# Kernel tuning notes

Measured on AMD Instinct MI355X. Metric: run time of the kernel, lower is better.

## Reference

```python
import jax, jax.numpy as jnp
import numpy as np


def setup_inputs() -> dict:
    key = jax.random.key(0)
    k1, k2, k3, k4 = jax.random.split(key, 4)
    B, S, IN, OUT = 2, 2048, 2048, 4096
    C, K, V = 128, 16, 16  # ncodebooks, ncentroids, vec_len
    return {
        "x": jax.random.normal(k1, (B, S, IN), dtype=jnp.float32),
        "weight": jax.random.normal(k2, (IN, OUT), dtype=jnp.float32) * 0.02,
        "centroids": jax.random.normal(k3, (C, K * V), dtype=jnp.float32),
        "bias": jax.random.normal(k4, (OUT,), dtype=jnp.float32) * 0.01,
        "vec_len": V,
    }


def reference(x, weight, centroids, bias, vec_len):
    B, S, IN = x.shape
    C = centroids.shape[0]            # ncodebooks
    V = vec_len
    K = centroids.shape[1] // V       # ncentroids
    OUT = weight.shape[1]
    N = B * S

    # [C, N, V] per-codebook token sub-vectors
    x_flat = jnp.transpose(x.reshape(N, C, V), (1, 0, 2))
    # [C, V, OUT] per-codebook weight slabs
    w_flat = weight.reshape(C, V, OUT)

    # soft path: sum_c x_c @ W_c  (fused contraction, no [C,N,OUT] intermediate)
    soft = jnp.einsum('cnv,cvo->no', x_flat, w_flat)

    # distance (p = inf -> Chebyshev) and nearest-centroid selection
    cents = centroids.reshape(C, K, V)
    dist = jnp.max(jnp.abs(x_flat[:, :, None, :] - cents[:, None, :, :]), axis=-1)  # [C,N,K]
    min_indices = jnp.argmin(dist, axis=-1)  # [C,N]

    # LUT: centroid outputs per codebook, then gather (== one_hot @ lut)
    lut = jnp.einsum('ckv,cvo->cko', cents, w_flat)  # [C,K,OUT]
    quant = jnp.sum(lut[jnp.arange(C)[:, None], min_indices], axis=0)  # [N,OUT]

    # straight-through estimator
    out = soft + jax.lax.stop_gradient(quant - soft)
    out = out.reshape(B, S, OUT) + bias
    return out
```

## Files before the change

### kernel.cpp

```cpp
#include <hip/hip_runtime.h>

typedef unsigned int u32;
typedef unsigned long long u64;
typedef __bf16 bf16x8 __attribute__((ext_vector_type(8)));
typedef float f32x4 __attribute__((ext_vector_type(4)));

#define N_TOK 4096
#define IN_DIM 2048
#define OUT_DIM 4096
#define NCB 128
#define NCENT 16
#define VLEN 16
#define CK 2048
#define KB 64

static __device__ __forceinline__ unsigned short f2bf(float f) {
  u32 u = __float_as_uint(f);
  u = (u + 0x7FFFu + ((u >> 16) & 1u)) >> 16;
  return (unsigned short)u;
}

__global__ __launch_bounds__(256) void k_argmin_idx(
    const float* __restrict__ x,
    const float* __restrict__ cents,
    unsigned char* __restrict__ idx) {
  __shared__ float xs[16 * 260];
  __shared__ float cs[16 * 260];
  const int tid = threadIdx.x;
  const int n0 = blockIdx.x * 16;
  const int t = tid >> 4;
  const int cl = tid & 15;

  for (int g = 0; g < 4; ++g) {
    const int cg = blockIdx.y * 4 + g;
#pragma unroll
    for (int j = 0; j < 4; ++j) {
      const int fi = tid + 256 * j;
      const int row = fi >> 6;
      const int col = (fi & 63) * 4;
      *(float4*)(xs + row * 260 + col) =
          *(const float4*)(x + (size_t)(n0 + row) * IN_DIM + cg * 256 + col);
      *(float4*)(cs + row * 260 + col) =
          *(const float4*)(cents + ((size_t)cg * 16 + row) * 256 + col);
    }
    __syncthreads();

    float xr[16];
    const float* xv = xs + t * 260 + cl * 16;
#pragma unroll
    for (int q = 0; q < 4; ++q) {
      float4 tv = *(const float4*)(xv + q * 4);
      xr[q * 4 + 0] = tv.x; xr[q * 4 + 1] = tv.y;
      xr[q * 4 + 2] = tv.z; xr[q * 4 + 3] = tv.w;
    }
    const float* cb = cs + cl * 260;
    int bk = 0;
    float bd = 1e30f;
#pragma unroll
    for (int k = 0; k < NCENT; ++k) {
      float d = 0.f;
#pragma unroll
      for (int v = 0; v < VLEN; ++v) d = fmaxf(d, fabsf(xr[v] - cb[k * 16 + v]));
      if (d < bd) { bd = d; bk = k; }
    }
    idx[(size_t)(n0 + t) * NCB + cg * 16 + cl] = (unsigned char)bk;
    __syncthreads();
  }
}

__global__ __launch_bounds__(256) void k_lut(const float* __restrict__ w,
                                             const float* __restrict__ cents,
                                             char* __restrict__ lutF) {
  const int tid = threadIdx.x;
  const int o0 = blockIdx.x * 64;
  const int cg = blockIdx.y;
  const int p = tid >> 6;
  const int ol = tid & 63;
  const int o = o0 + ol;

  float acc[2][16];
#pragma unroll
  for (int cc = 0; cc < 2; ++cc)
#pragma unroll
    for (int k = 0; k < 16; ++k) acc[cc][k] = 0.f;

#pragma unroll
  for (int cc = 0; cc < 2; ++cc) {
    const int c = __builtin_amdgcn_readfirstlane(cg * 8 + p * 2 + cc);
    const float* cb = cents + (size_t)c * (NCENT * VLEN);
#pragma unroll
    for (int v = 0; v < VLEN; ++v) {
      const float wv = w[(size_t)(c * 16 + v) * OUT_DIM + o];
#pragma unroll
      for (int k = 0; k < NCENT; ++k) acc[cc][k] = fmaf(cb[k * 16 + v], wv, acc[cc][k]);
    }
  }

#pragma unroll
  for (int cc = 0; cc < 2; ++cc) {
    const int c = cg * 8 + p * 2 + cc;
    u32 g[8];
#pragma unroll
    for (int kk = 0; kk < 8; ++kk)
      g[kk] = (u32)f2bf(acc[cc][2 * kk]) | ((u32)f2bf(acc[cc][2 * kk + 1]) << 16);
    char* base = lutF + ((size_t)(o >> 4) * KB + (c >> 1)) * 1024;
    const int l0 = (o & 15) + ((c & 1) * 2) * 16;
    *(uint4*)(base + l0 * 16)        = make_uint4(g[0], g[1], g[2], g[3]);
    *(uint4*)(base + (l0 + 16) * 16) = make_uint4(g[4], g[5], g[6], g[7]);
  }
}

__global__ __launch_bounds__(256) void k_gemm(
    const unsigned char* __restrict__ idx,
    const char* __restrict__ Bf,
    const float* __restrict__ bias,
    float* __restrict__ out) {
  __shared__ unsigned char sIdx[128 * 144];
  const int tid = threadIdx.x;
  const int wave = tid >> 6;
  const int lane = tid & 63;

  const int lin = blockIdx.x + (int)(gridDim.x * blockIdx.y);
  const int slot = lin >> 3;
  const int bx = slot & 31;
  const int by = ((lin & 7) << 2) | (slot >> 5);
  const int m0 = bx * 128;
  const int n0 = by * 128;
  const int wm = (wave >> 1) * 64;
  const int wn = (wave & 1) * 64;

#pragma unroll
  for (int j = 0; j < 4; ++j) {
    const int u = tid + 256 * j;
    const int row = u >> 3;
    const int col = (u & 7) * 16;
    *(uint4*)(sIdx + row * 144 + col) =
        *(const uint4*)(idx + (size_t)(m0 + row) * NCB + col);
  }

  const int h = lane >> 4;
  const int hb = h >> 1;
  const u32 par8 = (u32)((h & 1) * 8);
  const u32 sh0 = (u32)(hb * 8);
  const u32 sh1 = sh0 + 16;
  const unsigned char* rb[4];
#pragma unroll
  for (int i = 0; i < 4; ++i) rb[i] = sIdx + (wm + i * 16 + (lane & 15)) * 144;

  const int tb = (n0 >> 4) + (wn >> 4);
  u32 bo0 = (u32)tb * (KB * 1024) + (u32)lane * 16;
  u32 bo1 = bo0 + KB * 1024;
  u32 bo2 = bo1 + KB * 1024;
  u32 bo3 = bo2 + KB * 1024;

  __syncthreads();

  uint4 Bc0 = *(const uint4*)(Bf + bo0);
  uint4 Bc1 = *(const uint4*)(Bf + bo1);
  uint4 Bc2 = *(const uint4*)(Bf + bo2);
  uint4 Bc3 = *(const uint4*)(Bf + bo3);
  bo0 += 1024; bo1 += 1024; bo2 += 1024; bo3 += 1024;

  f32x4 acc[4][4] = {};

  for (int q = 0; q < 8; ++q) {
    uint4 ch[4];
#pragma unroll
    for (int i = 0; i < 4; ++i) ch[i] = *(const uint4*)(rb[i] + q * 16);

#pragma unroll
    for (int j = 0; j < 8; ++j) {
      uint4 Bn0 = *(const uint4*)(Bf + bo0);
      uint4 Bn1 = *(const uint4*)(Bf + bo1);
      uint4 Bn2 = *(const uint4*)(Bf + bo2);
      uint4 Bn3 = *(const uint4*)(Bf + bo3);
      bo0 += 1024; bo1 += 1024; bo2 += 1024; bo3 += 1024;

      const u32 sh = (j & 1) ? sh1 : sh0;
      bf16x8 af[4];
#pragma unroll
      for (int i = 0; i < 4; ++i) {
        const u32 word = (j >> 1) == 0 ? ch[i].x
                       : (j >> 1) == 1 ? ch[i].y
                       : (j >> 1) == 2 ? ch[i].z
                                       : ch[i].w;
        const u32 iv = (word >> sh) & 0xFu;
        const u32 uu = iv ^ par8;
        const u64 dbl = 0x3F80ull << ((uu & 3u) << 4);
        const u64 lo = ((uu & 12u) == 0u) ? dbl : 0ull;
        const u64 hi = ((uu & 12u) == 4u) ? dbl : 0ull;
        uint4 f;
        f.x = (u32)lo; f.y = (u32)(lo >> 32);
        f.z = (u32)hi; f.w = (u32)(hi >> 32);
        af[i] = *(bf16x8*)&f;
      }

#pragma unroll
      for (int i = 0; i < 4; ++i) {
        acc[i][0] = __builtin_amdgcn_mfma_f32_16x16x32_bf16(
            af[i], *(const bf16x8*)&Bc0, acc[i][0], 0, 0, 0);
        acc[i][1] = __builtin_amdgcn_mfma_f32_16x16x32_bf16(
            af[i], *(const bf16x8*)&Bc1, acc[i][1], 0, 0, 0);
        acc[i][2] = __builtin_amdgcn_mfma_f32_16x16x32_bf16(
            af[i], *(const bf16x8*)&Bc2, acc[i][2], 0, 0, 0);
        acc[i][3] = __builtin_amdgcn_mfma_f32_16x16x32_bf16(
            af[i], *(const bf16x8*)&Bc3, acc[i][3], 0, 0, 0);
      }

      Bc0 = Bn0; Bc1 = Bn1; Bc2 = Bn2; Bc3 = Bn3;
    }
  }

  const int col = lane & 15;
  const int rbq = (lane >> 4) * 4;
  float bj[4];
#pragma unroll
  for (int j = 0; j < 4; ++j) bj[j] = bias[n0 + wn + j * 16 + col];
#pragma unroll
  for (int i = 0; i < 4; ++i) {
    const int gm = m0 + wm + i * 16 + rbq;
#pragma unroll
    for (int j = 0; j < 4; ++j) {
      const int gn = n0 + wn + j * 16 + col;
      float* op = out + (size_t)gm * OUT_DIM + gn;
#pragma unroll
      for (int r = 0; r < 4; ++r) op[(size_t)r * OUT_DIM] = acc[i][j][r] + bj[j];
    }
  }
}

extern "C" void kernel_launch(void* const* d_in, const int* in_sizes, int n_in,
                              void* d_out, int out_size, void* d_ws, size_t ws_size,
                              hipStream_t stream) {
  (void)in_sizes; (void)n_in; (void)out_size; (void)ws_size;
  const float* x      = (const float*)d_in[0];
  const float* weight = (const float*)d_in[1];
  const float* cents  = (const float*)d_in[2];
  const float* bias   = (const float*)d_in[3];

  char* lutF = (char*)d_ws;
  unsigned char* idx = (unsigned char*)d_ws + (size_t)OUT_DIM * CK * 2;
  float* out = (float*)d_out;

  k_argmin_idx<<<dim3(N_TOK / 16, 2), 256, 0, stream>>>(x, cents, idx);
  k_lut<<<dim3(OUT_DIM / 64, NCB / 8), 256, 0, stream>>>(weight, cents, lutF);
  k_gemm<<<dim3(N_TOK / 128, OUT_DIM / 128), 256, 0, stream>>>(idx, lutF, bias, out);
}
```

Baseline: 190.2 us.

## Fuse LUT and argmin prep kernels, retile GEMM waves to 32x128 strips

Merges the LUT build and the nearest-centroid search into a single launch whose first 1024 blocks build the LUT and whose remaining blocks compute argmin indices. The argmin part now has each thread handle two tokens, reading x directly from global memory, and spreads the work over more blocks. The GEMM gives each wave a 32-row by 128-column strip instead of 64x64. This cuts per-wave one-hot A-fragment construction in half, moves the parity XOR out of the inner loop, and reuses each A fragment across 8 B tiles. The cost is more B-fragment registers and global loads per wave, which may lower occupancy.

```diff
diff --git a/kernel.cpp b/kernel.cpp
--- a/kernel.cpp
+++ b/kernel.cpp
@@ -20,94 +20,106 @@
   return (unsigned short)u;
 }
 
-__global__ __launch_bounds__(256) void k_argmin_idx(
+__global__ __launch_bounds__(256) void k_prep(
     const float* __restrict__ x,
+    const float* __restrict__ w,
     const float* __restrict__ cents,
-    unsigned char* __restrict__ idx) {
-  __shared__ float xs[16 * 260];
+    unsigned char* __restrict__ idx,
+    char* __restrict__ lutF) {
   __shared__ float cs[16 * 260];
   const int tid = threadIdx.x;
-  const int n0 = blockIdx.x * 16;
+  const int b = blockIdx.x;
+
+  if (b < 1024) {
+    const int o0 = (b & 63) * 64;
+    const int cg = b >> 6;
+    const int p = tid >> 6;
+    const int ol = tid & 63;
+    const int o = o0 + ol;
+
+    float acc[2][16];
+#pragma unroll
+    for (int cc = 0; cc < 2; ++cc)
+#pragma unroll
+      for (int k = 0; k < 16; ++k) acc[cc][k] = 0.f;
+
+#pragma unroll
+    for (int cc = 0; cc < 2; ++cc) {
+      const int c = __builtin_amdgcn_readfirstlane(cg * 8 + p * 2 + cc);
+      const float* cb = cents + (size_t)c * (NCENT * VLEN);
+#pragma unroll
+      for (int v = 0; v < VLEN; ++v) {
+        const float wv = w[(size_t)(c * 16 + v) * OUT_DIM + o];
+#pragma unroll
+        for (int k = 0; k < 16; ++k) acc[cc][k] = fmaf(cb[k * 16 + v], wv, acc[cc][k]);
+      }
+    }
+
+#pragma unroll
+    for (int cc = 0; cc < 2; ++cc) {
+      const int c = cg * 8 + p * 2 + cc;
+      u32 g[8];
+#pragma unroll
+      for (int kk = 0; kk < 8; ++kk)
+        g[kk] = (u32)f2bf(acc[cc][2 * kk]) | ((u32)f2bf(acc[cc][2 * kk + 1]) << 16);
+      char* base = lutF + ((size_t)(o >> 4) * KB + (c >> 1)) * 1024;
+      const int l0 = (o & 15) + ((c & 1) * 2) * 16;
+      *(uint4*)(base + l0 * 16)        = make_uint4(g[0], g[1], g[2], g[3]);
+      *(uint4*)(base + (l0 + 16) * 16) = make_uint4(g[4], g[5], g[6], g[7]);
+    }
+    return;
+  }
+
+  const int a = b - 1024;
+  const int n0 = (a & 127) * 32;
+  const int cg = a >> 7;
   const int t = tid >> 4;
   const int cl = tid & 15;
 
-  for (int g = 0; g < 4; ++g) {
-    const int cg = blockIdx.y * 4 + g;
-#pragma unroll
-    for (int j = 0; j < 4; ++j) {
-      const int fi = tid + 256 * j;
-      const int row = fi >> 6;
-      const int col = (fi & 63) * 4;
-      *(float4*)(xs + row * 260 + col) =
-          *(const float4*)(x + (size_t)(n0 + row) * IN_DIM + cg * 256 + col);
-      *(float4*)(cs + row * 260 + col) =
-          *(const float4*)(cents + ((size_t)cg * 16 + row) * 256 + col);
-    }
-    __syncthreads();
-
-    float xr[16];
-    const float* xv = xs + t * 260 + cl * 16;
-#pragma unroll
-    for (int q = 0; q < 4; ++q) {
-      float4 tv = *(const float4*)(xv + q * 4);
-      xr[q * 4 + 0] = tv.x; xr[q * 4 + 1] = tv.y;
-      xr[q * 4 + 2] = tv.z; xr[q * 4 + 3] = tv.w;
-    }
-    const float* cb = cs + cl * 260;
-    int bk = 0;
-    float bd = 1e30f;
-#pragma unroll
-    for (int k = 0; k < NCENT; ++k) {
-      float d = 0.f;
-#pragma unroll
-      for (int v = 0; v < VLEN; ++v) d = fmaxf(d, fabsf(xr[v] - cb[k * 16 + v]));
-      if (d < bd) { bd = d; bk = k; }
-    }
-    idx[(size_t)(n0 + t) * NCB + cg * 16 + cl] = (unsigned char)bk;
-    __syncthreads();
-  }
-}
-
-__global__ __launch_bounds__(256) void k_lut(const float* __restrict__ w,
-                                             const float* __restrict__ cents,
-                                             char* __restrict__ lutF) {
-  const int tid = threadIdx.x;
-  const int o0 = blockIdx.x * 64;
-  const int cg = blockIdx.y;
-  const int p = tid >> 6;
-  const int ol = tid & 63;
-  const int o = o0 + ol;
-
-  float acc[2][16];
-#pragma unroll
-  for (int cc = 0; cc < 2; ++cc)
-#pragma unroll
-    for (int k = 0; k < 16; ++k) acc[cc][k] = 0.f;
-
-#pragma unroll
-  for (int cc = 0; cc < 2; ++cc) {
-    const int c = __builtin_amdgcn_readfirstlane(cg * 8 + p * 2 + cc);
-    const float* cb = cents + (size_t)c * (NCENT * VLEN);
-#pragma unroll
-    for (int v = 0; v < VLEN; ++v) {
-      const float wv = w[(size_t)(c * 16 + v) * OUT_DIM + o];
-#pragma unroll
-      for (int k = 0; k < NCENT; ++k) acc[cc][k] = fmaf(cb[k * 16 + v], wv, acc[cc][k]);
-    }
-  }
-
-#pragma unroll
-  for (int cc = 0; cc < 2; ++cc) {
-    const int c = cg * 8 + p * 2 + cc;
-    u32 g[8];
-#pragma unroll
-    for (int kk = 0; kk < 8; ++kk)
-      g[kk] = (u32)f2bf(acc[cc][2 * kk]) | ((u32)f2bf(acc[cc][2 * kk + 1]) << 16);
-    char* base = lutF + ((size_t)(o >> 4) * KB + (c >> 1)) * 1024;
-    const int l0 = (o & 15) + ((c & 1) * 2) * 16;
-    *(uint4*)(base + l0 * 16)        = make_uint4(g[0], g[1], g[2], g[3]);
-    *(uint4*)(base + (l0 + 16) * 16) = make_uint4(g[4], g[5], g[6], g[7]);
-  }
+#pragma unroll
+  for (int j2 = 0; j2 < 4; ++j2) {
+    const int fi = tid + 256 * j2;
+    const int row = fi >> 6;
+    const int col = (fi & 63) * 4;
+    *(float4*)(cs + row * 260 + col) =
+        *(const float4*)(cents + ((size_t)(cg * 16 + row)) * 256 + col);
+  }
+
+  float xr[2][16];
+#pragma unroll
+  for (int s = 0; s < 2; ++s)
+#pragma unroll
+    for (int qq = 0; qq < 4; ++qq) {
+      float4 tv = *(const float4*)(x + (size_t)(n0 + t + 16 * s) * IN_DIM +
+                                   cg * 256 + cl * 16 + qq * 4);
+      xr[s][qq * 4 + 0] = tv.x; xr[s][qq * 4 + 1] = tv.y;
+      xr[s][qq * 4 + 2] = tv.z; xr[s][qq * 4 + 3] = tv.w;
+    }
+  __syncthreads();
+
+  const float* cb = cs + cl * 260;
+  int bk0 = 0, bk1 = 0;
+  float bd0 = 1e30f, bd1 = 1e30f;
+#pragma unroll
+  for (int k = 0; k < 16; ++k) {
+    float d0 = 0.f, d1 = 0.f;
+#pragma unroll
+    for (int qq = 0; qq < 4; ++qq) {
+      float4 cv = *(const float4*)(cb + k * 16 + qq * 4);
+      d0 = fmaxf(d0, fabsf(xr[0][qq * 4 + 0] - cv.x));
+      d0 = fmaxf(d0, fabsf(xr[0][qq * 4 + 1] - cv.y));
+      d0 = fmaxf(d0, fabsf(xr[0][qq * 4 + 2] - cv.z));
+      d0 = fmaxf(d0, fabsf(xr[0][qq * 4 + 3] - cv.w));
+      d1 = fmaxf(d1, fabsf(xr[1][qq * 4 + 0] - cv.x));
+      d1 = fmaxf(d1, fabsf(xr[1][qq * 4 + 1] - cv.y));
+      d1 = fmaxf(d1, fabsf(xr[1][qq * 4 + 2] - cv.z));
+      d1 = fmaxf(d1, fabsf(xr[1][qq * 4 + 3] - cv.w));
+    }
+    if (d0 < bd0) { bd0 = d0; bk0 = k; }
+    if (d1 < bd1) { bd1 = d1; bk1 = k; }
+  }
+  idx[(size_t)(n0 + t) * NCB + cg * 16 + cl] = (unsigned char)bk0;
+  idx[(size_t)(n0 + t + 16) * NCB + cg * 16 + cl] = (unsigned char)bk1;
 }
 
 __global__ __launch_bounds__(256) void k_gemm(
@@ -126,8 +138,7 @@
   const int by = ((lin & 7) << 2) | (slot >> 5);
   const int m0 = bx * 128;
   const int n0 = by * 128;
-  const int wm = (wave >> 1) * 64;
-  const int wn = (wave & 1) * 64;
+  const int wm = wave * 32;
 
 #pragma unroll
   for (int j = 0; j < 4; ++j) {
@@ -139,92 +150,87 @@
   }
 
   const int h = lane >> 4;
-  const int hb = h >> 1;
-  const u32 par8 = (u32)((h & 1) * 8);
-  const u32 sh0 = (u32)(hb * 8);
-  const u32 sh1 = sh0 + 16;
-  const unsigned char* rb[4];
-#pragma unroll
-  for (int i = 0; i < 4; ++i) rb[i] = sIdx + (wm + i * 16 + (lane & 15)) * 144;
-
-  const int tb = (n0 >> 4) + (wn >> 4);
-  u32 bo0 = (u32)tb * (KB * 1024) + (u32)lane * 16;
-  u32 bo1 = bo0 + KB * 1024;
-  u32 bo2 = bo1 + KB * 1024;
-  u32 bo3 = bo2 + KB * 1024;
+  const u32 sh_e = (u32)((h >> 1) * 8);
+  const u32 sh_o = sh_e + 16u;
+  const u32 pxor = (h & 1) ? 0x08080808u : 0u;
+  const unsigned char* rb0 = sIdx + (wm + (lane & 15)) * 144;
+  const unsigned char* rb1 = rb0 + 16 * 144;
+
+  u32 bo[8];
+#pragma unroll
+  for (int jj = 0; jj < 8; ++jj)
+    bo[jj] = (u32)(((n0 >> 4) + jj) * (KB * 1024)) + (u32)lane * 16u;
 
   __syncthreads();
 
-  uint4 Bc0 = *(const uint4*)(Bf + bo0);
-  uint4 Bc1 = *(const uint4*)(Bf + bo1);
-  uint4 Bc2 = *(const uint4*)(Bf + bo2);
-  uint4 Bc3 = *(const uint4*)(Bf + bo3);
-  bo0 += 1024; bo1 += 1024; bo2 += 1024; bo3 += 1024;
-
-  f32x4 acc[4][4] = {};
+  uint4 Bc[8];
+#pragma unroll
+  for (int jj = 0; jj < 8; ++jj) Bc[jj] = *(const uint4*)(Bf + bo[jj]);
+
+  f32x4 acc[2][8] = {};
 
   for (int q = 0; q < 8; ++q) {
-    uint4 ch[4];
-#pragma unroll
-    for (int i = 0; i < 4; ++i) ch[i] = *(const uint4*)(rb[i] + q * 16);
+    uint4 c0 = *(const uint4*)(rb0 + q * 16);
+    uint4 c1 = *(const uint4*)(rb1 + q * 16);
+    c0.x ^= pxor; c0.y ^= pxor; c0.z ^= pxor; c0.w ^= pxor;
+    c1.x ^= pxor; c1.y ^= pxor; c1.z ^= pxor; c1.w ^= pxor;
 
 #pragma unroll
     for (int j = 0; j < 8; ++j) {
-      uint4 Bn0 = *(const uint4*)(Bf + bo0);
-      uint4 Bn1 = *(const uint4*)(Bf + bo1);
-      uint4 Bn2 = *(const uint4*)(Bf + bo2);
-      uint4 Bn3 = *(const uint4*)(Bf + bo3);
-      bo0 += 1024; bo1 += 1024; bo2 += 1024; bo3 += 1024;
-
-      const u32 sh = (j & 1) ? sh1 : sh0;
-      bf16x8 af[4];
-#pragma unroll
-      for (int i = 0; i < 4; ++i) {
-        const u32 word = (j >> 1) == 0 ? ch[i].x
-                       : (j >> 1) == 1 ? ch[i].y
-                       : (j >> 1) == 2 ? ch[i].z
-                                       : ch[i].w;
-        const u32 iv = (word >> sh) & 0xFu;
-        const u32 uu = iv ^ par8;
-        const u64 dbl = 0x3F80ull << ((uu & 3u) << 4);
-        const u64 lo = ((uu & 12u) == 0u) ? dbl : 0ull;
-        const u64 hi = ((uu & 12u) == 4u) ? dbl : 0ull;
-        uint4 f;
-        f.x = (u32)lo; f.y = (u32)(lo >> 32);
-        f.z = (u32)hi; f.w = (u32)(hi >> 32);
-        af[i] = *(bf16x8*)&f;
+      uint4 Bn[8];
+#pragma unroll
+      for (int jj = 0; jj < 8; ++jj)
+        Bn[jj] = *(const uint4*)(Bf + (bo[jj] + (u32)((j + 1) * 1024)));
+
+      const u32 w0 = ((j >> 1) == 0 ? c0.x : (j >> 1) == 1 ? c0.y
+                     : (j >> 1) == 2 ? c0.z : c0.w);
+      const u32 w1 = ((j >> 1) == 0 ? c1.x : (j >> 1) == 1 ? c1.y
+                     : (j >> 1) == 2 ? c1.z : c1.w);
+      const u32 sh = (j & 1) ? sh_o : sh_e;
+      const u32 uu0 = (w0 >> sh) & 15u;
+      const u32 uu1 = (w1 >> sh) & 15u;
+      const u64 dbl0 = 0x3F80ull << ((uu0 << 4) & 63u);
+      const u64 dbl1 = 0x3F80ull << ((uu1 << 4) & 63u);
+      const u64 lo0 = (uu0 < 4u) ? dbl0 : 0ull;
+      const u64 hi0 = (uu0 >= 4u && uu0 < 8u) ? dbl0 : 0ull;
+      const u64 lo1 = (uu1 < 4u) ? dbl1 : 0ull;
+      const u64 hi1 = (uu1 >= 4u && uu1 < 8u) ? dbl1 : 0ull;
+      uint4 f0, f1;
+      f0.x = (u32)lo0; f0.y = (u32)(lo0 >> 32);
+      f0.z = (u32)hi0; f0.w = (u32)(hi0 >> 32);
+      f1.x = (u32)lo1; f1.y = (u32)(lo1 >> 32);
+      f1.z = (u32)hi1; f1.w = (u32)(hi1 >> 32);
+      const bf16x8 af0 = *(const bf16x8*)&f0;
+      const bf16x8 af1 = *(const bf16x8*)&f1;
+
+#pragma unroll
+      for (int jj = 0; jj < 8; ++jj) {
+        acc[0][jj] = __builtin_amdgcn_mfma_f32_16x16x32_bf16(
+            af0, *(const bf16x8*)&Bc[jj], acc[0][jj], 0, 0, 0);
+        acc[1][jj] = __builtin_amdgcn_mfma_f32_16x16x32_bf16(
+            af1, *(const bf16x8*)&Bc[jj], acc[1][jj], 0, 0, 0);
       }
 
 #pragma unroll
-      for (int i = 0; i < 4; ++i) {
-        acc[i][0] = __builtin_amdgcn_mfma_f32_16x16x32_bf16(
-            af[i], *(const bf16x8*)&Bc0, acc[i][0], 0, 0, 0);
-        acc[i][1] = __builtin_amdgcn_mfma_f32_16x16x32_bf16(
-            af[i], *(const bf16x8*)&Bc1, acc[i][1], 0, 0, 0);
-        acc[i][2] = __builtin_amdgcn_mfma_f32_16x16x32_bf16(
-            af[i], *(const bf16x8*)&Bc2, acc[i][2], 0, 0, 0);
-        acc[i][3] = __builtin_amdgcn_mfma_f32_16x16x32_bf16(
-            af[i], *(const bf16x8*)&Bc3, acc[i][3], 0, 0, 0);
-      }
-
-      Bc0 = Bn0; Bc1 = Bn1; Bc2 = Bn2; Bc3 = Bn3;
-    }
+      for (int jj = 0; jj < 8; ++jj) Bc[jj] = Bn[jj];
+    }
+#pragma unroll
+    for (int jj = 0; jj < 8; ++jj) bo[jj] += 8192u;
   }
 
   const int col = lane & 15;
-  const int rbq = (lane >> 4) * 4;
-  float bj[4];
-#pragma unroll
-  for (int j = 0; j < 4; ++j) bj[j] = bias[n0 + wn + j * 16 + col];
-#pragma unroll
-  for (int i = 0; i < 4; ++i) {
-    const int gm = m0 + wm + i * 16 + rbq;
-#pragma unroll
-    for (int j = 0; j < 4; ++j) {
-      const int gn = n0 + wn + j * 16 + col;
-      float* op = out + (size_t)gm * OUT_DIM + gn;
-#pragma unroll
-      for (int r = 0; r < 4; ++r) op[(size_t)r * OUT_DIM] = acc[i][j][r] + bj[j];
+  const int rq = (lane >> 4) * 4;
+  float bj[8];
+#pragma unroll
+  for (int jj = 0; jj < 8; ++jj) bj[jj] = bias[n0 + jj * 16 + col];
+#pragma unroll
+  for (int i = 0; i < 2; ++i) {
+    const int gm = m0 + wm + i * 16 + rq;
+#pragma unroll
+    for (int jj = 0; jj < 8; ++jj) {
+      float* op = out + (size_t)gm * OUT_DIM + n0 + jj * 16 + col;
+#pragma unroll
+      for (int r = 0; r < 4; ++r) op[(size_t)r * OUT_DIM] = acc[i][jj][r] + bj[jj];
     }
   }
 }
@@ -242,7 +248,6 @@
   unsigned char* idx = (unsigned char*)d_ws + (size_t)OUT_DIM * CK * 2;
   float* out = (float*)d_out;
 
-  k_argmin_idx<<<dim3(N_TOK / 16, 2), 256, 0, stream>>>(x, cents, idx);
-  k_lut<<<dim3(OUT_DIM / 64, NCB / 8), 256, 0, stream>>>(weight, cents, lutF);
-  k_gemm<<<dim3(N_TOK / 128, OUT_DIM / 128), 256, 0, stream>>>(idx, lutF, bias, out);
-}
+  k_prep<<<dim3(2048), 256, 0, stream>>>(x, weight, cents, idx, lutF);
+  k_gemm<<<dim3(32, 32), 256, 0, stream>>>(idx, lutF, bias, out);
+}
```

Result: slower. 206.0 us (+8.3%).

## Merge argmin and LUT kernels into one launch and simplify one-hot decode

Applied to the files above, without the earlier changes.

Combines the LUT-building kernel and the nearest-centroid argmin kernel into one launch using a block-index split, which removes one kernel launch and lets the two independent stages run concurrently. The argmin path now has each thread handle two tokens per codebook and reads x straight from global memory, so the x shared-memory staging is gone and more blocks run in parallel. In the GEMM, the parity XOR is applied once per loaded index word rather than on every decode, and the one-hot construction uses cheaper comparisons. The risk is load imbalance between the two block types sharing one grid.

```diff
diff --git a/kernel.cpp b/kernel.cpp
--- a/kernel.cpp
+++ b/kernel.cpp
@@ -20,94 +20,106 @@
   return (unsigned short)u;
 }
 
-__global__ __launch_bounds__(256) void k_argmin_idx(
+__global__ __launch_bounds__(256) void k_prep(
     const float* __restrict__ x,
+    const float* __restrict__ w,
     const float* __restrict__ cents,
-    unsigned char* __restrict__ idx) {
-  __shared__ float xs[16 * 260];
+    unsigned char* __restrict__ idx,
+    char* __restrict__ lutF) {
   __shared__ float cs[16 * 260];
   const int tid = threadIdx.x;
-  const int n0 = blockIdx.x * 16;
+  const int b = blockIdx.x;
+
+  if (b < 1024) {
+    const int o0 = (b & 63) * 64;
+    const int cg = b >> 6;
+    const int p = tid >> 6;
+    const int ol = tid & 63;
+    const int o = o0 + ol;
+
+    float acc[2][16];
+#pragma unroll
+    for (int cc = 0; cc < 2; ++cc)
+#pragma unroll
+      for (int k = 0; k < 16; ++k) acc[cc][k] = 0.f;
+
+#pragma unroll
+    for (int cc = 0; cc < 2; ++cc) {
+      const int c = __builtin_amdgcn_readfirstlane(cg * 8 + p * 2 + cc);
+      const float* cb = cents + (size_t)c * (NCENT * VLEN);
+#pragma unroll
+      for (int v = 0; v < VLEN; ++v) {
+        const float wv = w[(size_t)(c * 16 + v) * OUT_DIM + o];
+#pragma unroll
+        for (int k = 0; k < 16; ++k) acc[cc][k] = fmaf(cb[k * 16 + v], wv, acc[cc][k]);
+      }
+    }
+
+#pragma unroll
+    for (int cc = 0; cc < 2; ++cc) {
+      const int c = cg * 8 + p * 2 + cc;
+      u32 g[8];
+#pragma unroll
+      for (int kk = 0; kk < 8; ++kk)
+        g[kk] = (u32)f2bf(acc[cc][2 * kk]) | ((u32)f2bf(acc[cc][2 * kk + 1]) << 16);
+      char* base = lutF + ((size_t)(o >> 4) * KB + (c >> 1)) * 1024;
+      const int l0 = (o & 15) + ((c & 1) * 2) * 16;
+      *(uint4*)(base + l0 * 16)        = make_uint4(g[0], g[1], g[2], g[3]);
+      *(uint4*)(base + (l0 + 16) * 16) = make_uint4(g[4], g[5], g[6], g[7]);
+    }
+    return;
+  }
+
+  const int a = b - 1024;
+  const int n0 = (a & 127) * 32;
+  const int cg = a >> 7;
   const int t = tid >> 4;
   const int cl = tid & 15;
 
-  for (int g = 0; g < 4; ++g) {
-    const int cg = blockIdx.y * 4 + g;
-#pragma unroll
-    for (int j = 0; j < 4; ++j) {
-      const int fi = tid + 256 * j;
-      const int row = fi >> 6;
-      const int col = (fi & 63) * 4;
-      *(float4*)(xs + row * 260 + col) =
-          *(const float4*)(x + (size_t)(n0 + row) * IN_DIM + cg * 256 + col);
-      *(float4*)(cs + row * 260 + col) =
-          *(const float4*)(cents + ((size_t)cg * 16 + row) * 256 + col);
-    }
-    __syncthreads();
-
-    float xr[16];
-    const float* xv = xs + t * 260 + cl * 16;
-#pragma unroll
-    for (int q = 0; q < 4; ++q) {
-      float4 tv = *(const float4*)(xv + q * 4);
-      xr[q * 4 + 0] = tv.x; xr[q * 4 + 1] = tv.y;
-      xr[q * 4 + 2] = tv.z; xr[q * 4 + 3] = tv.w;
-    }
-    const float* cb = cs + cl * 260;
-    int bk = 0;
-    float bd = 1e30f;
-#pragma unroll
-    for (int k = 0; k < NCENT; ++k) {
-      float d = 0.f;
-#pragma unroll
-      for (int v = 0; v < VLEN; ++v) d = fmaxf(d, fabsf(xr[v] - cb[k * 16 + v]));
-      if (d < bd) { bd = d; bk = k; }
-    }
-    idx[(size_t)(n0 + t) * NCB + cg * 16 + cl] = (unsigned char)bk;
-    __syncthreads();
-  }
-}
-
-__global__ __launch_bounds__(256) void k_lut(const float* __restrict__ w,
-                                             const float* __restrict__ cents,
-                                             char* __restrict__ lutF) {
-  const int tid = threadIdx.x;
-  const int o0 = blockIdx.x * 64;
-  const int cg = blockIdx.y;
-  const int p = tid >> 6;
-  const int ol = tid & 63;
-  const int o = o0 + ol;
-
-  float acc[2][16];
-#pragma unroll
-  for (int cc = 0; cc < 2; ++cc)
-#pragma unroll
-    for (int k = 0; k < 16; ++k) acc[cc][k] = 0.f;
-
-#pragma unroll
-  for (int cc = 0; cc < 2; ++cc) {
-    const int c = __builtin_amdgcn_readfirstlane(cg * 8 + p * 2 + cc);
-    const float* cb = cents + (size_t)c * (NCENT * VLEN);
-#pragma unroll
-    for (int v = 0; v < VLEN; ++v) {
-      const float wv = w[(size_t)(c * 16 + v) * OUT_DIM + o];
-#pragma unroll
-      for (int k = 0; k < NCENT; ++k) acc[cc][k] = fmaf(cb[k * 16 + v], wv, acc[cc][k]);
-    }
-  }
-
-#pragma unroll
-  for (int cc = 0; cc < 2; ++cc) {
-    const int c = cg * 8 + p * 2 + cc;
-    u32 g[8];
-#pragma unroll
-    for (int kk = 0; kk < 8; ++kk)
-      g[kk] = (u32)f2bf(acc[cc][2 * kk]) | ((u32)f2bf(acc[cc][2 * kk + 1]) << 16);
-    char* base = lutF + ((size_t)(o >> 4) * KB + (c >> 1)) * 1024;
-    const int l0 = (o & 15) + ((c & 1) * 2) * 16;
-    *(uint4*)(base + l0 * 16)        = make_uint4(g[0], g[1], g[2], g[3]);
-    *(uint4*)(base + (l0 + 16) * 16) = make_uint4(g[4], g[5], g[6], g[7]);
-  }
+#pragma unroll
+  for (int j2 = 0; j2 < 4; ++j2) {
+    const int fi = tid + 256 * j2;
+    const int row = fi >> 6;
+    const int col = (fi & 63) * 4;
+    *(float4*)(cs + row * 260 + col) =
+        *(const float4*)(cents + ((size_t)(cg * 16 + row)) * 256 + col);
+  }
+
+  float xr[2][16];
+#pragma unroll
+  for (int s = 0; s < 2; ++s)
+#pragma unroll
+    for (int qq = 0; qq < 4; ++qq) {
+      float4 tv = *(const float4*)(x + (size_t)(n0 + t + 16 * s) * IN_DIM +
+                                   cg * 256 + cl * 16 + qq * 4);
+      xr[s][qq * 4 + 0] = tv.x; xr[s][qq * 4 + 1] = tv.y;
+      xr[s][qq * 4 + 2] = tv.z; xr[s][qq * 4 + 3] = tv.w;
+    }
+  __syncthreads();
+
+  const float* cb = cs + cl * 260;
+  int bk0 = 0, bk1 = 0;
+  float bd0 = 1e30f, bd1 = 1e30f;
+#pragma unroll
+  for (int k = 0; k < 16; ++k) {
+    float d0 = 0.f, d1 = 0.f;
+#pragma unroll
+    for (int qq = 0; qq < 4; ++qq) {
+      float4 cv = *(const float4*)(cb + k * 16 + qq * 4);
+      d0 = fmaxf(d0, fabsf(xr[0][qq * 4 + 0] - cv.x));
+      d0 = fmaxf(d0, fabsf(xr[0][qq * 4 + 1] - cv.y));
+      d0 = fmaxf(d0, fabsf(xr[0][qq * 4 + 2] - cv.z));
+      d0 = fmaxf(d0, fabsf(xr[0][qq * 4 + 3] - cv.w));
+      d1 = fmaxf(d1, fabsf(xr[1][qq * 4 + 0] - cv.x));
+      d1 = fmaxf(d1, fabsf(xr[1][qq * 4 + 1] - cv.y));
+      d1 = fmaxf(d1, fabsf(xr[1][qq * 4 + 2] - cv.z));
+      d1 = fmaxf(d1, fabsf(xr[1][qq * 4 + 3] - cv.w));
+    }
+    if (d0 < bd0) { bd0 = d0; bk0 = k; }
+    if (d1 < bd1) { bd1 = d1; bk1 = k; }
+  }
+  idx[(size_t)(n0 + t) * NCB + cg * 16 + cl] = (unsigned char)bk0;
+  idx[(size_t)(n0 + t + 16) * NCB + cg * 16 + cl] = (unsigned char)bk1;
 }
 
 __global__ __launch_bounds__(256) void k_gemm(
@@ -139,16 +151,15 @@
   }
 
   const int h = lane >> 4;
-  const int hb = h >> 1;
-  const u32 par8 = (u32)((h & 1) * 8);
-  const u32 sh0 = (u32)(hb * 8);
-  const u32 sh1 = sh0 + 16;
+  const u32 sh_e = (u32)((h >> 1) * 8);
+  const u32 sh_o = sh_e + 16u;
+  const u32 pxor = (h & 1) ? 0x08080808u : 0u;
   const unsigned char* rb[4];
 #pragma unroll
   for (int i = 0; i < 4; ++i) rb[i] = sIdx + (wm + i * 16 + (lane & 15)) * 144;
 
   const int tb = (n0 >> 4) + (wn >> 4);
-  u32 bo0 = (u32)tb * (KB * 1024) + (u32)lane * 16;
+  u32 bo0 = (u32)(tb + 0) * (KB * 1024) + (u32)lane * 16;
   u32 bo1 = bo0 + KB * 1024;
   u32 bo2 = bo1 + KB * 1024;
   u32 bo3 = bo2 + KB * 1024;
@@ -166,7 +177,10 @@
   for (int q = 0; q < 8; ++q) {
     uint4 ch[4];
 #pragma unroll
-    for (int i = 0; i < 4; ++i) ch[i] = *(const uint4*)(rb[i] + q * 16);
+    for (int i = 0; i < 4; ++i) {
+      ch[i] = *(const uint4*)(rb[i] + q * 16);
+      ch[i].x ^= pxor; ch[i].y ^= pxor; ch[i].z ^= pxor; ch[i].w ^= pxor;
+    }
 
 #pragma unroll
     for (int j = 0; j < 8; ++j) {
@@ -176,7 +190,7 @@
       uint4 Bn3 = *(const uint4*)(Bf + bo3);
       bo0 += 1024; bo1 += 1024; bo2 += 1024; bo3 += 1024;
 
-      const u32 sh = (j & 1) ? sh1 : sh0;
+      const u32 sh = (j & 1) ? sh_o : sh_e;
       bf16x8 af[4];
 #pragma unroll
       for (int i = 0; i < 4; ++i) {
@@ -184,11 +198,11 @@
                        : (j >> 1) == 1 ? ch[i].y
                        : (j >> 1) == 2 ? ch[i].z
                                        : ch[i].w;
-        const u32 iv = (word >> sh) & 0xFu;
-        const u32 uu = iv ^ par8;
-        const u64 dbl = 0x3F80ull << ((uu & 3u) << 4);
-        const u64 lo = ((uu & 12u) == 0u) ? dbl : 0ull;
-        const u64 hi = ((uu & 12u) == 4u) ? dbl : 0ull;
+        const u32 uu = (word >> sh) & 15u;
+        const u32 sa = (uu << 4) & 63u;
+        const u64 dbl = 0x3F80ull << sa;
+        const u64 lo = (uu < 4u) ? dbl : 0ull;
+        const u64 hi = ((uu - 4u) < 4u) ? dbl : 0ull;
         uint4 f;
         f.x = (u32)lo; f.y = (u32)(lo >> 32);
         f.z = (u32)hi; f.w = (u32)(hi >> 32);
@@ -212,13 +226,13 @@
   }
 
   const int col = lane & 15;
-  const int rbq = (lane >> 4) * 4;
+  const int rq = (lane >> 4) * 4;
   float bj[4];
 #pragma unroll
   for (int j = 0; j < 4; ++j) bj[j] = bias[n0 + wn + j * 16 + col];
 #pragma unroll
   for (int i = 0; i < 4; ++i) {
-    const int gm = m0 + wm + i * 16 + rbq;
+    const int gm = m0 + wm + i * 16 + rq;
 #pragma unroll
     for (int j = 0; j < 4; ++j) {
       const int gn = n0 + wn + j * 16 + col;
@@ -242,7 +256,6 @@
   unsigned char* idx = (unsigned char*)d_ws + (size_t)OUT_DIM * CK * 2;
   float* out = (float*)d_out;
 
-  k_argmin_idx<<<dim3(N_TOK / 16, 2), 256, 0, stream>>>(x, cents, idx);
-  k_lut<<<dim3(OUT_DIM / 64, NCB / 8), 256, 0, stream>>>(weight, cents, lutF);
-  k_gemm<<<dim3(N_TOK / 128, OUT_DIM / 128), 256, 0, stream>>>(idx, lutF, bias, out);
-}
+  k_prep<<<dim3(2048), 256, 0, stream>>>(x, weight, cents, idx, lutF);
+  k_gemm<<<dim3(32, 32), 256, 0, stream>>>(idx, lutF, bias, out);
+}
```

Measured after the change: 172.1 us (median of 3 runs). -9.5%, faster.
